# Kernel optimization log

Hardware: AMD Instinct MI355X
Metric: run time of the kernel (lower is better)

The kernel has to match this reference:

```python
import jax, jax.numpy as jnp
import numpy as np

BATCH = 64
INPUT_LENGTH = 128
N_TERMINALS = 64
N_NONTERMINALS = 128


def setup_inputs() -> dict:
    key = jax.random.key(0)
    k1, k2, k3 = jax.random.split(key, 3)
    input_tensor = jax.random.uniform(k1, (BATCH, INPUT_LENGTH, N_TERMINALS), dtype=jnp.float32)
    terminal_productions = jax.random.normal(k2, (N_NONTERMINALS, N_TERMINALS), dtype=jnp.float32)
    nonterminal_productions = jax.random.normal(k3, (N_NONTERMINALS, N_NONTERMINALS, N_TERMINALS), dtype=jnp.float32)
    return {
        "input_tensor": input_tensor,
        "terminal_productions": terminal_productions,
        "nonterminal_productions": nonterminal_productions,
    }


def reference(input_tensor, terminal_productions, nonterminal_productions):
    # input_tensor: [B, L, T]
    tp = jax.nn.sigmoid(terminal_productions)            # [N, T]
    ntp = jax.nn.sigmoid(nonterminal_productions)        # [N, N, T]

    # step 0: terminal production choices
    tpc = jnp.einsum('nt,bt->bn', tp, input_tensor[:, 0])  # [B, N]
    out0 = tpc[:, 0]                                        # [B]

    def step(carry, x_i):
        prev_choices, prev_out = carry                     # [B, N], [B]
        # per-batch nonterminal production choice matrix: [B, N, N]
        npc = jnp.clip(jnp.einsum('nmt,bt->bnm', ntp, x_i), 0.0, 1.0)
        cur = jnp.clip(jnp.einsum('bnm,bm->bn', npc, prev_choices), 0.0, 1.0)
        mask = x_i[:, N_TERMINALS - 1]                     # [B]
        out = prev_out * mask + cur[:, 0] * (1.0 - mask)
        return (cur, out), None

    xs = jnp.swapaxes(input_tensor[:, 1:], 0, 1)           # [L-1, B, T]
    (final_choices, final_out), _ = jax.lax.scan(step, (tpc, out0), xs)
    return final_out[:, None]                              # [B, 1]
```

## Files before the change

kernel.cpp:

```cpp
#include <hip/hip_runtime.h>
#include <hip/hip_bf16.h>

typedef unsigned int u32;
typedef unsigned char u8;
typedef _Float16 f16;
typedef f16 f16x2 __attribute__((ext_vector_type(2)));
typedef short s16x8 __attribute__((ext_vector_type(8)));
typedef float f32x4 __attribute__((ext_vector_type(4)));

#define BB 64
#define LL 128
#define TT 64
#define NN 128
#define NM (NN*NN)

__device__ __forceinline__ float sigf(float v) {
    return 1.0f / (1.0f + __expf(-v));
}

__device__ __forceinline__ float clip01(float v) {
    return fminf(fmaxf(v, 0.f), 1.f);
}

__device__ __forceinline__ u32 f2bf(float f) {
    u32 u = __builtin_bit_cast(u32, f);
    return (u + 0x7fffu + ((u >> 16) & 1u)) >> 16;
}

__device__ __forceinline__ float fdot2f(f16x2 wa, f16x2 xa, float ca) {
#if defined(__HIP_DEVICE_COMPILE__) && __has_builtin(__builtin_amdgcn_fdot2)
    return __builtin_amdgcn_fdot2(wa, xa, ca, false);
#else
    return ca + (float)wa[0] * (float)xa[0] + (float)wa[1] * (float)xa[1];
#endif
}

__device__ __forceinline__ u32 ud4(u32 a, u32 b, u32 c) {
#if defined(__HIP_DEVICE_COMPILE__) && __has_builtin(__builtin_amdgcn_udot4)
    return __builtin_amdgcn_udot4(a, b, c, false);
#else
    return c + (a & 255u) * (b & 255u) + ((a >> 8) & 255u) * ((b >> 8) & 255u)
             + ((a >> 16) & 255u) * ((b >> 16) & 255u) + (a >> 24) * (b >> 24);
#endif
}

__global__ __launch_bounds__(256) void pack_wx(const float* __restrict__ ntp,
                                               const float* __restrict__ x_all,
                                               ushort* __restrict__ wpk,
                                               ushort* __restrict__ xpk) {
    const int bid = blockIdx.x;
    if (bid < 512) {
        const int g = bid * 256 + threadIdx.x;
        const int l = g & 63, h = (g >> 6) & 1, i = g >> 7;
        const int row = i * 16 + (l & 15);
        const int t0 = h * 32 + ((l >> 4) << 3);
        const float* src = ntp + row * 64 + t0;
        float4 f0 = *reinterpret_cast<const float4*>(src);
        float4 f1 = *reinterpret_cast<const float4*>(src + 4);
        float v[8] = {f0.x, f0.y, f0.z, f0.w, f1.x, f1.y, f1.z, f1.w};
        u32 o[4];
        #pragma unroll
        for (int q = 0; q < 4; ++q)
            o[q] = f2bf(sigf(v[2 * q])) | (f2bf(sigf(v[2 * q + 1])) << 16);
        uint4 ov; ov.x = o[0]; ov.y = o[1]; ov.z = o[2]; ov.w = o[3];
        *reinterpret_cast<uint4*>(wpk + (size_t)g * 8) = ov;
    } else {
        const int g = (bid - 512) * 256 + threadIdx.x;
        const int l = g & 63, h = (g >> 6) & 1, j = (g >> 7) & 7, b = g >> 10;
        const int s = j * 16 + (l & 15);
        const int t0 = h * 32 + ((l >> 4) << 3);
        const float* src = x_all + ((size_t)b * LL + s) * TT + t0;
        float4 f0 = *reinterpret_cast<const float4*>(src);
        float4 f1 = *reinterpret_cast<const float4*>(src + 4);
        float v[8] = {f0.x, f0.y, f0.z, f0.w, f1.x, f1.y, f1.z, f1.w};
        u32 o[4];
        #pragma unroll
        for (int q = 0; q < 4; ++q)
            o[q] = f2bf(v[2 * q]) | (f2bf(v[2 * q + 1]) << 16);
        uint4 ov; ov.x = o[0]; ov.y = o[1]; ov.z = o[2]; ov.w = o[3];
        *reinterpret_cast<uint4*>(xpk + (size_t)g * 8) = ov;
    }
}

__global__ __launch_bounds__(256) void gemm_mfma(const ushort* __restrict__ wpk,
                                                 const ushort* __restrict__ xpk,
                                                 u8* __restrict__ npc) {
    __shared__ __align__(16) u8 stg[4][8192];
    const int b = blockIdx.x >> 4;
    const int nb = blockIdx.x & 15;
    const int wv = threadIdx.x >> 6, l = threadIdx.x & 63;

    uint4 xf[8][2];
    #pragma unroll
    for (int j = 0; j < 8; ++j)
        #pragma unroll
        for (int h = 0; h < 2; ++h)
            xf[j][h] = *reinterpret_cast<const uint4*>(
                xpk + (size_t)(((b * 8 + j) * 2 + h) * 64 + l) * 8);

    const int c = l & 15, r0 = (l >> 4) * 4;
    u8* stw = stg[wv];
    const int khi  = (nb >> 3) * 8;
    const int nlow = (nb & 7) * 8;

    for (int mg2 = 0; mg2 < 2; ++mg2) {
        const int mg = wv * 2 + mg2;
        #pragma unroll
        for (int n_l = 0; n_l < 8; ++n_l) {
            const int i = (nb * 8 + n_l) * 8 + mg;
            uint4 a0 = *reinterpret_cast<const uint4*>(wpk + (size_t)((i * 2 + 0) * 64 + l) * 8);
            uint4 a1 = *reinterpret_cast<const uint4*>(wpk + (size_t)((i * 2 + 1) * 64 + l) * 8);
            const f32x4 z = {0.f, 0.f, 0.f, 0.f};
            f32x4 acc[8];
            #pragma unroll
            for (int j = 0; j < 8; ++j)
                acc[j] = __builtin_amdgcn_mfma_f32_16x16x32_bf16(
                    __builtin_bit_cast(s16x8, a0), __builtin_bit_cast(s16x8, xf[j][0]), z, 0, 0, 0);
            #pragma unroll
            for (int j = 0; j < 8; ++j)
                acc[j] = __builtin_amdgcn_mfma_f32_16x16x32_bf16(
                    __builtin_bit_cast(s16x8, a1), __builtin_bit_cast(s16x8, xf[j][1]), acc[j], 0, 0, 0);

            const int sk8 = ((n_l + c) & 7) << 3;
            #pragma unroll
            for (int j = 0; j < 8; ++j) {
                u32 q0 = (u32)(clip01(acc[j][0]) * 15.f + 0.5f);
                u32 q1 = (u32)(clip01(acc[j][1]) * 15.f + 0.5f);
                u32 q2 = (u32)(clip01(acc[j][2]) * 15.f + 0.5f);
                u32 q3 = (u32)(clip01(acc[j][3]) * 15.f + 0.5f);
                u32 hw = (q0 | (q1 << 4)) | ((q2 | (q3 << 4)) << 8);
                *reinterpret_cast<ushort*>(stw + j * 1024 + c * 64 + sk8 + (r0 >> 1)) = (ushort)hw;
            }
        }
        asm volatile("s_waitcnt lgkmcnt(0)" ::: "memory");
        __builtin_amdgcn_sched_barrier(0);

        #pragma unroll
        for (int j = 0; j < 8; ++j) {
            #pragma unroll
            for (int r = 0; r < 2; ++r) {
                const int slot = r * 64 + l;
                const int cc = slot >> 3;
                const int nr = slot & 7;
                uint2 v = *reinterpret_cast<const uint2*>(
                    stw + j * 1024 + cc * 64 + (((nr + cc) & 7) << 3));
                *reinterpret_cast<uint2*>(npc + ((size_t)b << 20) + ((size_t)j << 17)
                    + ((size_t)cc << 13) + ((size_t)(mg + khi) << 9)
                    + ((nlow + nr) << 3)) = v;
            }
        }
        asm volatile("s_waitcnt lgkmcnt(0)" ::: "memory");
        __builtin_amdgcn_sched_barrier(0);
    }
}

__global__ __launch_bounds__(256, 1) void recur9(const float* __restrict__ x_all,
                                                 const float* __restrict__ tp,
                                                 const u8* __restrict__ npc,
                                                 float* __restrict__ outp) {
    __shared__ u32 prev_pk[2][32];
    __shared__ float masks_lds[LL];
    __shared__ float tpc_lds[NN];
    __shared__ float x0_lds[TT];

    const int b = blockIdx.x, tid = threadIdx.x;
    const int n = tid >> 1, h = tid & 1;
    const u8* npcl = npc + ((size_t)b << 20)
                   + ((size_t)((n >> 6) * 8 + h * 4) << 9) + (u32)(n & 63) * 8;

    if (tid < 128) masks_lds[tid] = x_all[(size_t)b * 8192 + tid * 64 + 63];
    else if (tid < 192) x0_lds[tid - 128] = x_all[(size_t)b * 8192 + (tid - 128)];
    __syncthreads();

#define LOADSET(R, T) do { \
        int _t = (T) <= 127 ? (T) : 127; \
        const u8* _p = npcl + ((size_t)(_t >> 4) << 17) + ((size_t)(_t & 15) << 13); \
        R[0] = *reinterpret_cast<const uint2*>(_p); \
        R[1] = *reinterpret_cast<const uint2*>(_p + 512); \
        R[2] = *reinterpret_cast<const uint2*>(_p + 1024); \
        R[3] = *reinterpret_cast<const uint2*>(_p + 1536); \
        asm volatile("" ::: "memory"); \
    } while (0)

    uint2 nA[4], nB[4], nC[4], nD[4];
    LOADSET(nA, 1); LOADSET(nB, 2); LOADSET(nC, 3); LOADSET(nD, 4);

    float out_r = 0.f;
    if (tid < 128) {
        float a = 0.f;
        #pragma unroll
        for (int t4 = 0; t4 < 16; ++t4) {
            float4 xv = *reinterpret_cast<const float4*>(x0_lds + t4 * 4);
            float4 w0 = *reinterpret_cast<const float4*>(tp + tid * 64 + t4 * 4);
            a += sigf(w0.x) * xv.x; a += sigf(w0.y) * xv.y;
            a += sigf(w0.z) * xv.z; a += sigf(w0.w) * xv.w;
        }
        tpc_lds[tid] = a;
        if (tid == 0) out_r = a;
    }
    asm volatile("s_waitcnt lgkmcnt(0)" ::: "memory");
    __builtin_amdgcn_s_barrier();
    __builtin_amdgcn_sched_barrier(0);

    const int wr_idx  = ((n >> 4) << 1) + ((n >> 3) & 1) + ((n & 1) << 4);
    const int wr_byte = (n & 7) >> 1;

    {
        float sf = 0.f;
        #pragma unroll
        for (int kk = 0; kk < 4; ++kk) {
            const int base_m = (4 * h + kk) * 16;
            u32 wlo = nA[kk].x, whi = nA[kk].y;
            #pragma unroll
            for (int by = 0; by < 4; ++by) {
                u32 b0 = (wlo >> (8 * by)) & 0xFFu;
                sf += (float)(b0 & 15u) * tpc_lds[base_m + 2 * by];
                sf += (float)(b0 >> 4)  * tpc_lds[base_m + 2 * by + 1];
                u32 b1 = (whi >> (8 * by)) & 0xFFu;
                sf += (float)(b1 & 15u) * tpc_lds[base_m + 8 + 2 * by];
                sf += (float)(b1 >> 4)  * tpc_lds[base_m + 8 + 2 * by + 1];
            }
        }
        float tot = sf + __shfl_xor(sf, 1);
        float c0 = clip01(tot * (1.f / 15.f));
        if (h == 0) {
            u32 q8 = (u32)(c0 * 255.f + 0.5f);
            ((u8*)&prev_pk[0][wr_idx])[wr_byte] = (u8)q8;
        }
        if (tid == 0) {
            float mk = masks_lds[1];
            out_r = out_r * mk + c0 * (1.f - mk);
        }
        asm volatile("s_waitcnt lgkmcnt(0)" ::: "memory");
        __builtin_amdgcn_s_barrier();
        __builtin_amdgcn_sched_barrier(0);
    }
    LOADSET(nA, 5);

    int p = 0;

#define STEP(R, S) do { \
        uint4 pe0 = *reinterpret_cast<const uint4*>(&prev_pk[p][8 * h]); \
        uint4 pe1 = *reinterpret_cast<const uint4*>(&prev_pk[p][8 * h + 4]); \
        uint4 po0 = *reinterpret_cast<const uint4*>(&prev_pk[p][16 + 8 * h]); \
        uint4 po1 = *reinterpret_cast<const uint4*>(&prev_pk[p][16 + 8 * h + 4]); \
        u32 PE[8] = {pe0.x, pe0.y, pe0.z, pe0.w, pe1.x, pe1.y, pe1.z, pe1.w}; \
        u32 PO[8] = {po0.x, po0.y, po0.z, po0.w, po1.x, po1.y, po1.z, po1.w}; \
        float mk = masks_lds[(S)]; \
        u32 ae = 0, ao = 0; \
        _Pragma("unroll") \
        for (int _kk = 0; _kk < 4; ++_kk) { \
            u32 _w0 = R[_kk].x, _w1 = R[_kk].y; \
            ae = ud4(_w0 & 0x0F0F0F0Fu, PE[2 * _kk], ae); \
            ao = ud4((_w0 >> 4) & 0x0F0F0F0Fu, PO[2 * _kk], ao); \
            ae = ud4(_w1 & 0x0F0F0F0Fu, PE[2 * _kk + 1], ae); \
            ao = ud4((_w1 >> 4) & 0x0F0F0F0Fu, PO[2 * _kk + 1], ao); \
        } \
        float sf = (float)(ae + ao); \
        float tot = sf + __shfl_xor(sf, 1); \
        float c0 = fminf(tot * (1.f / 3825.f), 1.f); \
        if (h == 0) { \
            u32 q8 = (u32)(c0 * 255.f + 0.5f); \
            ((u8*)&prev_pk[p ^ 1][wr_idx])[wr_byte] = (u8)q8; \
        } \
        if (tid == 0) out_r = out_r * mk + c0 * (1.f - mk); \
        asm volatile("s_waitcnt lgkmcnt(0)" ::: "memory"); \
        __builtin_amdgcn_s_barrier(); \
        __builtin_amdgcn_sched_barrier(0); \
        p ^= 1; \
    } while (0)

    for (int g = 0; g < 31; ++g) {
        const int s = 2 + 4 * g;
        STEP(nB, s);     LOADSET(nB, s + 4);
        STEP(nC, s + 1); LOADSET(nC, s + 5);
        STEP(nD, s + 2); LOADSET(nD, s + 6);
        STEP(nA, s + 3); LOADSET(nA, s + 7);
    }
    STEP(nB, 126);
    STEP(nC, 127);

#undef STEP
#undef LOADSET

    if (tid == 0) outp[b] = out_r;
}

__global__ __launch_bounds__(256) void sig_transpose(const float* __restrict__ ntp,
                                                     u32* __restrict__ out) {
    __shared__ float lds[64 * 65];
    const int nm0 = blockIdx.x * 64;
    const int tid = threadIdx.x;
    #pragma unroll
    for (int it = 0; it < 16; ++it) {
        int idx = it * 256 + tid;
        int r = idx >> 6, c = idx & 63;
        lds[r * 65 + c] = sigf(ntp[(nm0 + r) * 64 + c]);
    }
    __syncthreads();
    #pragma unroll
    for (int it = 0; it < 8; ++it) {
        int o = it * 256 + tid;
        int tpi = o >> 6, r = o & 63;
        f16x2 h;
        h[0] = (f16)lds[r * 65 + 2 * tpi];
        h[1] = (f16)lds[r * 65 + 2 * tpi + 1];
        out[tpi * NM + nm0 + r] = __builtin_bit_cast(u32, h);
    }
}

__global__ __launch_bounds__(1024) void grammar_fused(
    const float* __restrict__ x_all,
    const float* __restrict__ tp,
    const u32*  __restrict__ ntpT2,
    float* __restrict__ outp) {
    __shared__ float x_lds[LL * TT];
    __shared__ float prevbuf[2][NN];
    __shared__ u32 x2_lds[2][32];

    const int b = blockIdx.x;
    const int tid = threadIdx.x;
    const int lane16 = tid & 15;
    const int g = tid >> 4;
    const int mbase = lane16 * 8;

    const float* xb = x_all + b * (LL * TT);
    #pragma unroll
    for (int it = 0; it < 8; ++it) {
        int idx = it * 1024 + tid;
        x_lds[idx] = xb[idx];
    }
    __syncthreads();

    if (tid < NN) {
        float acc = 0.f;
        #pragma unroll 8
        for (int t = 0; t < TT; ++t)
            acc += sigf(tp[tid * TT + t]) * x_lds[t];
        prevbuf[0][tid] = acc;
    }
    __syncthreads();
    float out_r = 0.f;
    if (tid == 0) out_r = prevbuf[0][0];

    int p = 0;
    for (int i0 = 1; i0 < LL; i0 += 2) {
        const int ns = (LL - i0) >= 2 ? 2 : 1;
        if (tid < 64) {
            int s = tid >> 5, tpi = tid & 31;
            f16x2 h;
            if (s < ns) {
                h[0] = (f16)x_lds[(i0 + s) * TT + 2 * tpi];
                h[1] = (f16)x_lds[(i0 + s) * TT + 2 * tpi + 1];
            } else {
                h[0] = (f16)0.f; h[1] = (f16)0.f;
            }
            x2_lds[s][tpi] = __builtin_bit_cast(u32, h);
        }
        __syncthreads();

        float acc[2][2][8];
        #pragma unroll
        for (int k = 0; k < 2; ++k)
            #pragma unroll
            for (int s = 0; s < 2; ++s)
                #pragma unroll
                for (int j = 0; j < 8; ++j) acc[k][s][j] = 0.f;

        #pragma unroll 2
        for (int tpi = 0; tpi < 32; ++tpi) {
            f16x2 xv0 = __builtin_bit_cast(f16x2, x2_lds[0][tpi]);
            f16x2 xv1 = __builtin_bit_cast(f16x2, x2_lds[1][tpi]);
            const u32* base = ntpT2 + tpi * NM + 8 * tid;
            #pragma unroll
            for (int k = 0; k < 2; ++k) {
                uint4 w0 = *reinterpret_cast<const uint4*>(base + 8192 * k);
                uint4 w1 = *reinterpret_cast<const uint4*>(base + 8192 * k + 4);
                u32 wv[8] = {w0.x, w0.y, w0.z, w0.w, w1.x, w1.y, w1.z, w1.w};
                #pragma unroll
                for (int j = 0; j < 8; ++j) {
                    f16x2 w = __builtin_bit_cast(f16x2, wv[j]);
                    acc[k][0][j] = fdot2f(w, xv0, acc[k][0][j]);
                    acc[k][1][j] = fdot2f(w, xv1, acc[k][1][j]);
                }
            }
        }

        for (int s = 0; s < ns; ++s) {
            float4 pv0 = *reinterpret_cast<const float4*>(&prevbuf[p][mbase]);
            float4 pv1 = *reinterpret_cast<const float4*>(&prevbuf[p][mbase + 4]);
            float pvv[8] = {pv0.x, pv0.y, pv0.z, pv0.w, pv1.x, pv1.y, pv1.z, pv1.w};
            #pragma unroll
            for (int k = 0; k < 2; ++k) {
                float part = 0.f;
                #pragma unroll
                for (int j = 0; j < 8; ++j) {
                    float npcv = clip01(acc[k][s][j]);
                    part += npcv * pvv[j];
                }
                part += __shfl_xor(part, 1);
                part += __shfl_xor(part, 2);
                part += __shfl_xor(part, 4);
                part += __shfl_xor(part, 8);
                if (lane16 == 0) {
                    float c = clip01(part);
                    prevbuf[p ^ 1][g + 64 * k] = c;
                    if (tid == 0 && k == 0) {
                        float mask = x_lds[(i0 + s) * TT + 63];
                        out_r = out_r * mask + c * (1.f - mask);
                    }
                }
            }
            p ^= 1;
            __syncthreads();
        }
    }

    if (tid == 0) outp[b] = out_r;
}

extern "C" void kernel_launch(void* const* d_in, const int* in_sizes, int n_in,
                              void* d_out, int out_size, void* d_ws, size_t ws_size,
                              hipStream_t stream) {
    const float* input_tensor = (const float*)d_in[0];
    const float* term_prod    = (const float*)d_in[1];
    const float* nonterm_prod = (const float*)d_in[2];
    float* outp = (float*)d_out;

    const size_t MB = 1024 * 1024;
    const size_t NPC_BYTES = 64 * MB;
    const size_t WPK_BYTES = 2 * MB;
    const size_t XPK_BYTES = 1 * MB;

    if (ws_size >= NPC_BYTES + WPK_BYTES + XPK_BYTES + MB) {
        u8* npcbuf  = (u8*)d_ws;
        ushort* wpk = (ushort*)((char*)d_ws + NPC_BYTES);
        ushort* xpk = (ushort*)((char*)d_ws + NPC_BYTES + WPK_BYTES);
        pack_wx<<<768, 256, 0, stream>>>(nonterm_prod, input_tensor, wpk, xpk);
        gemm_mfma<<<1024, 256, 0, stream>>>(wpk, xpk, npcbuf);
        recur9<<<BB, 256, 0, stream>>>(input_tensor, term_prod, npcbuf, outp);
    } else {
        u32* ntpT2 = (u32*)d_ws;
        sig_transpose<<<256, 256, 0, stream>>>(nonterm_prod, ntpT2);
        grammar_fused<<<BB, 1024, 0, stream>>>(input_tensor, term_prod, ntpT2, outp);
    }
}
```

Baseline: 77.77 us.

## Fuse GEMM and recurrence into one kernel with per-batch flag handoff

Merges the MFMA kernel that builds the per-batch choice matrices and the sequential recurrence kernel into a single launch. GEMM blocks write their npc slices and signal per-batch, per-half atomic counters. Recurrence blocks spin on these counters, so a batch can start its first half of the steps while the second half is still being computed. This targets the launch gap and the serial dependency between the two stages. In exchange it relies on the spinning consumer blocks not starving producer blocks of compute units, and uses a bounded spin as a deadlock guard.

```diff
diff --git a/kernel.cpp b/kernel.cpp
--- a/kernel.cpp
+++ b/kernel.cpp
@@ -47,8 +47,10 @@
 __global__ __launch_bounds__(256) void pack_wx(const float* __restrict__ ntp,
                                                const float* __restrict__ x_all,
                                                ushort* __restrict__ wpk,
-                                               ushort* __restrict__ xpk) {
+                                               ushort* __restrict__ xpk,
+                                               u32* __restrict__ flags) {
     const int bid = blockIdx.x;
+    if (bid == 0 && threadIdx.x < 128) flags[threadIdx.x] = 0u;
     if (bid < 512) {
         const int g = bid * 256 + threadIdx.x;
         const int l = g & 63, h = (g >> 6) & 1, i = g >> 7;
@@ -82,91 +84,117 @@
     }
 }
 
-__global__ __launch_bounds__(256) void gemm_mfma(const ushort* __restrict__ wpk,
-                                                 const ushort* __restrict__ xpk,
-                                                 u8* __restrict__ npc) {
-    __shared__ __align__(16) u8 stg[4][8192];
-    const int b = blockIdx.x >> 4;
-    const int nb = blockIdx.x & 15;
-    const int wv = threadIdx.x >> 6, l = threadIdx.x & 63;
-
-    uint4 xf[8][2];
-    #pragma unroll
-    for (int j = 0; j < 8; ++j)
-        #pragma unroll
-        for (int h = 0; h < 2; ++h)
-            xf[j][h] = *reinterpret_cast<const uint4*>(
-                xpk + (size_t)(((b * 8 + j) * 2 + h) * 64 + l) * 8);
-
-    const int c = l & 15, r0 = (l >> 4) * 4;
-    u8* stw = stg[wv];
-    const int khi  = (nb >> 3) * 8;
-    const int nlow = (nb & 7) * 8;
-
-    for (int mg2 = 0; mg2 < 2; ++mg2) {
-        const int mg = wv * 2 + mg2;
-        #pragma unroll
-        for (int n_l = 0; n_l < 8; ++n_l) {
-            const int i = (nb * 8 + n_l) * 8 + mg;
-            uint4 a0 = *reinterpret_cast<const uint4*>(wpk + (size_t)((i * 2 + 0) * 64 + l) * 8);
-            uint4 a1 = *reinterpret_cast<const uint4*>(wpk + (size_t)((i * 2 + 1) * 64 + l) * 8);
-            const f32x4 z = {0.f, 0.f, 0.f, 0.f};
-            f32x4 acc[8];
-            #pragma unroll
-            for (int j = 0; j < 8; ++j)
-                acc[j] = __builtin_amdgcn_mfma_f32_16x16x32_bf16(
-                    __builtin_bit_cast(s16x8, a0), __builtin_bit_cast(s16x8, xf[j][0]), z, 0, 0, 0);
-            #pragma unroll
-            for (int j = 0; j < 8; ++j)
-                acc[j] = __builtin_amdgcn_mfma_f32_16x16x32_bf16(
-                    __builtin_bit_cast(s16x8, a1), __builtin_bit_cast(s16x8, xf[j][1]), acc[j], 0, 0, 0);
-
-            const int sk8 = ((n_l + c) & 7) << 3;
-            #pragma unroll
-            for (int j = 0; j < 8; ++j) {
-                u32 q0 = (u32)(clip01(acc[j][0]) * 15.f + 0.5f);
-                u32 q1 = (u32)(clip01(acc[j][1]) * 15.f + 0.5f);
-                u32 q2 = (u32)(clip01(acc[j][2]) * 15.f + 0.5f);
-                u32 q3 = (u32)(clip01(acc[j][3]) * 15.f + 0.5f);
-                u32 hw = (q0 | (q1 << 4)) | ((q2 | (q3 << 4)) << 8);
-                *reinterpret_cast<ushort*>(stw + j * 1024 + c * 64 + sk8 + (r0 >> 1)) = (ushort)hw;
-            }
-        }
-        asm volatile("s_waitcnt lgkmcnt(0)" ::: "memory");
-        __builtin_amdgcn_sched_barrier(0);
-
-        #pragma unroll
-        for (int j = 0; j < 8; ++j) {
-            #pragma unroll
-            for (int r = 0; r < 2; ++r) {
-                const int slot = r * 64 + l;
-                const int cc = slot >> 3;
-                const int nr = slot & 7;
-                uint2 v = *reinterpret_cast<const uint2*>(
-                    stw + j * 1024 + cc * 64 + (((nr + cc) & 7) << 3));
-                *reinterpret_cast<uint2*>(npc + ((size_t)b << 20) + ((size_t)j << 17)
-                    + ((size_t)cc << 13) + ((size_t)(mg + khi) << 9)
-                    + ((nlow + nr) << 3)) = v;
-            }
-        }
-        asm volatile("s_waitcnt lgkmcnt(0)" ::: "memory");
-        __builtin_amdgcn_sched_barrier(0);
-    }
-}
-
-__global__ __launch_bounds__(256, 1) void recur9(const float* __restrict__ x_all,
-                                                 const float* __restrict__ tp,
-                                                 const u8* __restrict__ npc,
-                                                 float* __restrict__ outp) {
+__global__ __launch_bounds__(256, 1) void mega(const float* __restrict__ x_all,
+                                               const float* __restrict__ tp,
+                                               const ushort* __restrict__ wpk,
+                                               const ushort* __restrict__ xpk,
+                                               u8* __restrict__ npc,
+                                               u32* __restrict__ flags,
+                                               float* __restrict__ outp) {
+    __shared__ __align__(16) u8 stg[4][4096];
     __shared__ u32 prev_pk[2][32];
     __shared__ float masks_lds[LL];
     __shared__ float tpc_lds[NN];
     __shared__ float x0_lds[TT];
 
-    const int b = blockIdx.x, tid = threadIdx.x;
+    const int bid = blockIdx.x;
+    const int tid = threadIdx.x;
+
+    if (bid < 1024) {
+        const int jh  = bid >> 9;
+        const int rem = bid & 511;
+        const int b   = rem >> 3;
+        const int nb8 = rem & 7;
+        const int wv = tid >> 6, l = tid & 63;
+
+        uint4 xf[4][2];
+        #pragma unroll
+        for (int jl = 0; jl < 4; ++jl)
+            #pragma unroll
+            for (int h = 0; h < 2; ++h)
+                xf[jl][h] = *reinterpret_cast<const uint4*>(
+                    xpk + (size_t)(((b * 8 + (jh * 4 + jl)) * 2 + h) * 64 + l) * 8);
+
+        const int c = l & 15, r0 = (l >> 4) * 4;
+        u8* stw = stg[wv];
+
+        for (int nh = 0; nh < 2; ++nh) {
+            const int nb = nb8 * 2 + nh;
+            const int khi  = (nb >> 3) * 8;
+            const int nlow = (nb & 7) * 8;
+            for (int mg2 = 0; mg2 < 2; ++mg2) {
+                const int mg = wv * 2 + mg2;
+                #pragma unroll
+                for (int n_l = 0; n_l < 8; ++n_l) {
+                    const int i = (nb * 8 + n_l) * 8 + mg;
+                    uint4 a0 = *reinterpret_cast<const uint4*>(wpk + (size_t)((i * 2 + 0) * 64 + l) * 8);
+                    uint4 a1 = *reinterpret_cast<const uint4*>(wpk + (size_t)((i * 2 + 1) * 64 + l) * 8);
+                    const f32x4 z = {0.f, 0.f, 0.f, 0.f};
+                    f32x4 acc[4];
+                    #pragma unroll
+                    for (int jl = 0; jl < 4; ++jl)
+                        acc[jl] = __builtin_amdgcn_mfma_f32_16x16x32_bf16(
+                            __builtin_bit_cast(s16x8, a0), __builtin_bit_cast(s16x8, xf[jl][0]), z, 0, 0, 0);
+                    #pragma unroll
+                    for (int jl = 0; jl < 4; ++jl)
+                        acc[jl] = __builtin_amdgcn_mfma_f32_16x16x32_bf16(
+                            __builtin_bit_cast(s16x8, a1), __builtin_bit_cast(s16x8, xf[jl][1]), acc[jl], 0, 0, 0);
+
+                    const int sk8 = ((n_l + c) & 7) << 3;
+                    #pragma unroll
+                    for (int jl = 0; jl < 4; ++jl) {
+                        u32 q0 = (u32)(clip01(acc[jl][0]) * 15.f + 0.5f);
+                        u32 q1 = (u32)(clip01(acc[jl][1]) * 15.f + 0.5f);
+                        u32 q2 = (u32)(clip01(acc[jl][2]) * 15.f + 0.5f);
+                        u32 q3 = (u32)(clip01(acc[jl][3]) * 15.f + 0.5f);
+                        u32 hw = (q0 | (q1 << 4)) | ((q2 | (q3 << 4)) << 8);
+                        *reinterpret_cast<ushort*>(stw + jl * 1024 + c * 64 + sk8 + (r0 >> 1)) = (ushort)hw;
+                    }
+                }
+                asm volatile("s_waitcnt lgkmcnt(0)" ::: "memory");
+                __builtin_amdgcn_sched_barrier(0);
+
+                #pragma unroll
+                for (int jl = 0; jl < 4; ++jl) {
+                    #pragma unroll
+                    for (int r = 0; r < 2; ++r) {
+                        const int slot = r * 64 + l;
+                        const int cc = slot >> 3;
+                        const int nr = slot & 7;
+                        uint2 v = *reinterpret_cast<const uint2*>(
+                            stw + jl * 1024 + cc * 64 + (((nr + cc) & 7) << 3));
+                        *reinterpret_cast<uint2*>(npc + ((size_t)b << 20)
+                            + ((size_t)(jh * 4 + jl) << 17)
+                            + ((size_t)cc << 13) + ((size_t)(mg + khi) << 9)
+                            + ((nlow + nr) << 3)) = v;
+                    }
+                }
+                asm volatile("s_waitcnt lgkmcnt(0)" ::: "memory");
+                __builtin_amdgcn_sched_barrier(0);
+            }
+        }
+
+        asm volatile("s_waitcnt vmcnt(0)" ::: "memory");
+        __syncthreads();
+        if (tid == 0) {
+            __threadfence();
+            atomicAdd(&flags[b * 2 + jh], 1u);
+        }
+        return;
+    }
+
+    const int b = bid - 1024;
     const int n = tid >> 1, h = tid & 1;
     const u8* npcl = npc + ((size_t)b << 20)
                    + ((size_t)((n >> 6) * 8 + h * 4) << 9) + (u32)(n & 63) * 8;
+
+    {
+        u32* f = &flags[b * 2];
+        int guard = 0;
+        while (atomicAdd(f, 0u) < 8u && ++guard < (1 << 20))
+            __builtin_amdgcn_s_sleep(8);
+        __threadfence();
+    }
 
     if (tid < 128) masks_lds[tid] = x_all[(size_t)b * 8192 + tid * 64 + 63];
     else if (tid < 192) x0_lds[tid - 128] = x_all[(size_t)b * 8192 + (tid - 128)];
@@ -270,7 +298,21 @@
         p ^= 1; \
     } while (0)
 
-    for (int g = 0; g < 31; ++g) {
+    for (int g = 0; g < 14; ++g) {
+        const int s = 2 + 4 * g;
+        STEP(nB, s);     LOADSET(nB, s + 4);
+        STEP(nC, s + 1); LOADSET(nC, s + 5);
+        STEP(nD, s + 2); LOADSET(nD, s + 6);
+        STEP(nA, s + 3); LOADSET(nA, s + 7);
+    }
+    {
+        u32* f = &flags[b * 2 + 1];
+        int guard = 0;
+        while (atomicAdd(f, 0u) < 8u && ++guard < (1 << 20))
+            __builtin_amdgcn_s_sleep(8);
+        __threadfence();
+    }
+    for (int g = 14; g < 31; ++g) {
         const int s = 2 + 4 * g;
         STEP(nB, s);     LOADSET(nB, s + 4);
         STEP(nC, s + 1); LOADSET(nC, s + 5);
@@ -431,14 +473,16 @@
     const size_t NPC_BYTES = 64 * MB;
     const size_t WPK_BYTES = 2 * MB;
     const size_t XPK_BYTES = 1 * MB;
-
-    if (ws_size >= NPC_BYTES + WPK_BYTES + XPK_BYTES + MB) {
+    const size_t FLG_BYTES = 512;
+
+    if (ws_size >= NPC_BYTES + WPK_BYTES + XPK_BYTES + FLG_BYTES + MB) {
         u8* npcbuf  = (u8*)d_ws;
         ushort* wpk = (ushort*)((char*)d_ws + NPC_BYTES);
         ushort* xpk = (ushort*)((char*)d_ws + NPC_BYTES + WPK_BYTES);
-        pack_wx<<<768, 256, 0, stream>>>(nonterm_prod, input_tensor, wpk, xpk);
-        gemm_mfma<<<1024, 256, 0, stream>>>(wpk, xpk, npcbuf);
-        recur9<<<BB, 256, 0, stream>>>(input_tensor, term_prod, npcbuf, outp);
+        u32* flags  = (u32*)((char*)d_ws + NPC_BYTES + WPK_BYTES + XPK_BYTES);
+        pack_wx<<<768, 256, 0, stream>>>(nonterm_prod, input_tensor, wpk, xpk, flags);
+        mega<<<1088, 256, 0, stream>>>(input_tensor, term_prod, wpk, xpk,
+                                       npcbuf, flags, outp);
     } else {
         u32* ntpT2 = (u32*)d_ws;
         sig_transpose<<<256, 256, 0, stream>>>(nonterm_prod, ntpT2);
```

New measurement: 133.5 us. +71.7%, slower.
